# Optimization experiments

Hardware: AMD Instinct MI355X
Metric: run time of the kernel (lower is better)

The kernel has to match this reference:

```python
import jax, jax.numpy as jnp
import numpy as np

B, S, H, NH, L, INTER, WIN = 2, 2048, 512, 8, 4, 2048, 64
HD = H // NH
W1 = WIN // 2          # one-sided window
WB = 2 * W1 + 1        # band width per query
EPS = 1e-12


def layer_norm(x, g, b):
    m = jnp.mean(x, axis=-1, keepdims=True)
    v = jnp.var(x, axis=-1, keepdims=True)
    return (x - m) / jnp.sqrt(v + EPS) * g + b


def setup_inputs() -> dict:
    key = jax.random.key(0)
    ks = jax.random.split(key, 12)
    std = 0.02
    n = lambda k, sh: jax.random.normal(k, sh, jnp.float32) * std
    return {
        "input_embs": jax.random.normal(ks[0], (B, S, H), jnp.float32),
        "attention_mask": jnp.ones((B, S), jnp.float32),
        "pos_emb": n(ks[1], (S, H)),
        "ln_emb_g": jnp.ones((H,), jnp.float32),
        "ln_emb_b": jnp.zeros((H,), jnp.float32),
        "Wq": n(ks[2], (L, H, H)), "bq": jnp.zeros((L, H), jnp.float32),
        "Wk": n(ks[3], (L, H, H)), "bk": jnp.zeros((L, H), jnp.float32),
        "Wv": n(ks[4], (L, H, H)), "bv": jnp.zeros((L, H), jnp.float32),
        "Wo": n(ks[5], (L, H, H)), "bo": jnp.zeros((L, H), jnp.float32),
        "ln1_g": jnp.ones((L, H), jnp.float32), "ln1_b": jnp.zeros((L, H), jnp.float32),
        "Wi": n(ks[6], (L, H, INTER)), "bi": jnp.zeros((L, INTER), jnp.float32),
        "Wo2": n(ks[7], (L, INTER, H)), "bo2": jnp.zeros((L, H), jnp.float32),
        "ln2_g": jnp.ones((L, H), jnp.float32), "ln2_b": jnp.zeros((L, H), jnp.float32),
        "pool_W1": n(ks[8], (H, H)), "pool_b1": jnp.zeros((H,), jnp.float32),
        "pool_W2": n(ks[9], (H, 1)), "pool_b2": jnp.zeros((1,), jnp.float32),
    }


def reference(input_embs, attention_mask, pos_emb, ln_emb_g, ln_emb_b,
              Wq, bq, Wk, bk, Wv, bv, Wo, bo, ln1_g, ln1_b,
              Wi, bi, Wo2, bo2, ln2_g, ln2_b,
              pool_W1, pool_b1, pool_W2, pool_b2):
    # extended additive mask: 0 for attend, -10000 for pad (no global tokens)
    ext = (1.0 - attention_mask) * -10000.0          # [B,S]
    is_masked = ext < 0                              # masked query positions

    # embeddings: input + position, LayerNorm (dropout is identity in eval)
    x = layer_norm(input_embs + pos_emb[None], ln_emb_g, ln_emb_b)

    # sliding-window band indices
    offs = jnp.arange(-W1, W1 + 1)
    idx = jnp.arange(S)[:, None] + offs[None, :]     # [S,WB]
    valid = (idx >= 0) & (idx < S)
    idxc = jnp.clip(idx, 0, S - 1)
    key_bias = ext[:, idxc]                          # [B,S,WB] additive key mask
    scale = 1.0 / jnp.sqrt(jnp.float32(HD))

    def layer(h, p):
        (wq, bq_, wk, bk_, wv, bv_, wo, bo_, g1, b1,
         wi, bi_, wo2, bo2_, g2, b2) = p
        q = (h @ wq + bq_).reshape(B, S, NH, HD) * scale
        k = (h @ wk + bk_).reshape(B, S, NH, HD)
        v = (h @ wv + bv_).reshape(B, S, NH, HD)
        kb = k[:, idxc]                              # [B,S,WB,NH,HD]
        vb = v[:, idxc]
        sc = jnp.einsum('bshd,bswhd->bhsw', q, kb) + key_bias[:, None]
        sc = jnp.where(valid[None, None], sc, -jnp.inf)
        pr = jax.nn.softmax(sc, axis=-1)
        pr = jnp.where(is_masked[:, None, :, None], 0.0, pr)
        ctx = jnp.einsum('bhsw,bswhd->bshd', pr, vb).reshape(B, S, H)
        attn = layer_norm(ctx @ wo + bo_ + h, g1, b1)          # BertSelfOutput
        inter = jax.nn.gelu(attn @ wi + bi_, approximate=False)  # BertIntermediate
        out = layer_norm(inter @ wo2 + bo2_ + attn, g2, b2)      # BertOutput
        return out, None

    params = (Wq, bq, Wk, bk, Wv, bv, Wo, bo, ln1_g, ln1_b,
              Wi, bi, Wo2, bo2, ln2_g, ln2_b)
    x, _ = jax.lax.scan(jax.checkpoint(layer), x, params)

    # AttentionPooling
    e = jnp.tanh(x @ pool_W1 + pool_b1)
    alpha = jnp.exp(e @ pool_W2 + pool_b2) * attention_mask[..., None]  # [B,S,1]
    alpha = alpha / (jnp.sum(alpha, axis=1, keepdims=True) + 1e-8)
    return jnp.einsum('bsh,bs->bh', x, alpha[..., 0])  # [B,H]
```

## Files before the change

### kernel.cpp

```cpp
#include <hip/hip_runtime.h>
#include <hip/hip_bf16.h>
#include <math.h>

#define B_ 2
#define S_ 2048
#define H_ 512
#define NH_ 8
#define HD_ 64
#define L_ 4
#define INTER_ 2048
#define W1_ 32
#define WB_ 65
#define M_ (B_*S_)

typedef __attribute__((ext_vector_type(8))) short short8v;
typedef __attribute__((ext_vector_type(4))) float f32x4;

__device__ __forceinline__ float b2f(ushort u){ return __uint_as_float(((unsigned)u)<<16); }
__device__ __forceinline__ ushort f2b(float f){
  unsigned u = __float_as_uint(f);
  unsigned r = (u + 0x7fffu + ((u>>16)&1u)) >> 16;
  return (ushort)r;
}

__device__ __forceinline__ void async16(const ushort* g, ushort* l){
  __builtin_amdgcn_global_load_lds(
      (const __attribute__((address_space(1))) unsigned int*)g,
      (__attribute__((address_space(3))) unsigned int*)l, 16, 0, 0);
}

__global__ __launch_bounds__(256) void transpose_k(const float* __restrict__ src,
    ushort* __restrict__ dst, int R, int C, size_t sBatch, size_t dBatch)
{
  __shared__ ushort tile[32][33];
  src += (size_t)blockIdx.z * sBatch;
  dst += (size_t)blockIdx.z * dBatch;
  int tx = threadIdx.x & 31, ty = threadIdx.x >> 5;
  int r0 = blockIdx.y * 32, c0 = blockIdx.x * 32;
  #pragma unroll
  for (int i = 0; i < 4; ++i){
    int r = r0 + ty + i*8;
    tile[ty + i*8][tx] = f2b(src[(size_t)r * C + c0 + tx]);
  }
  __syncthreads();
  #pragma unroll
  for (int i = 0; i < 4; ++i){
    int c = c0 + ty + i*8;
    dst[(size_t)c * R + r0 + tx] = tile[tx][ty + i*8];
  }
}

__global__ __launch_bounds__(256) void pack_bqkv(const float* __restrict__ bq,
    const float* __restrict__ bk, const float* __restrict__ bv, float* __restrict__ dst)
{
  int i = blockIdx.x * 256 + threadIdx.x;
  int l = i / 1536, n = i % 1536;
  float v = (n < 512) ? bq[l*512 + n] : (n < 1024 ? bk[l*512 + n - 512] : bv[l*512 + n - 1024]);
  dst[i] = v;
}

template<int EPI>
__global__ __launch_bounds__(256, 4) void gemm_bt(
    const ushort* __restrict__ A, const ushort* __restrict__ Bt,
    const float* __restrict__ bias, ushort* __restrict__ o16,
    float* __restrict__ o32, int M, int N, int K)
{
  __shared__ ushort lds_a[64][32];
  __shared__ ushort lds_b[128][32];
  const int tid = threadIdx.x;
  const int bm = blockIdx.y * 64, bn = blockIdx.x * 128;
  const int wave = tid >> 6, lane = tid & 63;
  const int wr = (wave >> 1) * 32, wc = (wave & 1) * 64;
  const int lr = lane & 15, lg = lane >> 4, lk = lg * 8;
  f32x4 acc[2][4] = {};

  const int srow = tid >> 2, schk = (tid & 3) * 8;
  const ushort* Ag  = A  + (size_t)(bm + srow) * K + schk;
  const ushort* Bg0 = Bt + (size_t)(bn + srow) * K + schk;
  const ushort* Bg1 = Bt + (size_t)(bn + 64 + srow) * K + schk;
  ushort* la  = &lds_a[0][0] + tid * 8;
  ushort* lb0 = &lds_b[0][0] + tid * 8;
  ushort* lb1 = &lds_b[64][0] + tid * 8;

  for (int k0 = 0; k0 < K; k0 += 32){
    __syncthreads();
    async16(Ag  + k0, la);
    async16(Bg0 + k0, lb0);
    async16(Bg1 + k0, lb1);
    __syncthreads();
    short8v af[2], bfr[4];
    #pragma unroll
    for (int mi = 0; mi < 2; ++mi)
      af[mi] = *(const short8v*)(&lds_a[wr + mi*16 + lr][lk]);
    #pragma unroll
    for (int nj = 0; nj < 4; ++nj)
      bfr[nj] = *(const short8v*)(&lds_b[wc + nj*16 + lr][lk]);
    #pragma unroll
    for (int mi = 0; mi < 2; ++mi)
      #pragma unroll
      for (int nj = 0; nj < 4; ++nj)
        acc[mi][nj] = __builtin_amdgcn_mfma_f32_16x16x32_bf16(af[mi], bfr[nj], acc[mi][nj], 0, 0, 0);
  }

  #pragma unroll
  for (int mi = 0; mi < 2; ++mi){
    #pragma unroll
    for (int nj = 0; nj < 4; ++nj){
      int col = bn + wc + nj*16 + lr;
      float bv = bias[col];
      #pragma unroll
      for (int j = 0; j < 4; ++j){
        int row = bm + wr + mi*16 + lg*4 + j;
        float v = acc[mi][nj][j] + bv;
        if (EPI == 1) v = 0.5f * v * (1.0f + erff(v * 0.70710678118654752f));
        if (EPI == 2) v = tanhf(v);
        if (EPI == 3) o32[(size_t)row * N + col] = v;
        else          o16[(size_t)row * N + col] = f2b(v);
      }
    }
  }
}

__device__ __forceinline__ void block_ln_stats(float v0, float v1, float* red,
                                               float& mean, float& rstd)
{
  int tid = threadIdx.x, wave = tid >> 6, lane = tid & 63;
  float sm = v0 + v1;
  float sq = v0*v0 + v1*v1;
  #pragma unroll
  for (int o = 32; o > 0; o >>= 1){ sm += __shfl_xor(sm, o); sq += __shfl_xor(sq, o); }
  if (lane == 0){ red[wave] = sm; red[4 + wave] = sq; }
  __syncthreads();
  float S = red[0] + red[1] + red[2] + red[3];
  float Q = red[4] + red[5] + red[6] + red[7];
  mean = S * (1.0f / 512.0f);
  float var = Q * (1.0f / 512.0f) - mean*mean;
  if (var < 0.f) var = 0.f;
  rstd = rsqrtf(var + 1e-12f);
}

__global__ __launch_bounds__(256) void embed_ln(const float* __restrict__ x,
    const float* __restrict__ pos, const float* __restrict__ g,
    const float* __restrict__ bb, ushort* __restrict__ out16, float* __restrict__ out32)
{
  __shared__ float red[8];
  int row = blockIdx.x, tid = threadIdx.x;
  int s = row & (S_ - 1);
  float v0 = x[(size_t)row*H_ + tid]       + pos[(size_t)s*H_ + tid];
  float v1 = x[(size_t)row*H_ + tid + 256] + pos[(size_t)s*H_ + tid + 256];
  float mean, rstd;
  block_ln_stats(v0, v1, red, mean, rstd);
  float r0 = (v0 - mean)*rstd*g[tid]       + bb[tid];
  float r1 = (v1 - mean)*rstd*g[tid + 256] + bb[tid + 256];
  out16[(size_t)row*H_ + tid]       = f2b(r0);
  out16[(size_t)row*H_ + tid + 256] = f2b(r1);
  out32[(size_t)row*H_ + tid]       = r0;
  out32[(size_t)row*H_ + tid + 256] = r1;
}

__global__ __launch_bounds__(256) void ln_res(const float* __restrict__ t,
    const float* __restrict__ res, const float* __restrict__ g,
    const float* __restrict__ bb, ushort* __restrict__ out16, float* __restrict__ out32)
{
  __shared__ float red[8];
  int row = blockIdx.x, tid = threadIdx.x;
  float v0 = t[(size_t)row*H_ + tid]       + res[(size_t)row*H_ + tid];
  float v1 = t[(size_t)row*H_ + tid + 256] + res[(size_t)row*H_ + tid + 256];
  float mean, rstd;
  block_ln_stats(v0, v1, red, mean, rstd);
  float r0 = (v0 - mean)*rstd*g[tid]       + bb[tid];
  float r1 = (v1 - mean)*rstd*g[tid + 256] + bb[tid + 256];
  out16[(size_t)row*H_ + tid]       = f2b(r0);
  out16[(size_t)row*H_ + tid + 256] = f2b(r1);
  out32[(size_t)row*H_ + tid]       = r0;
  out32[(size_t)row*H_ + tid + 256] = r1;
}

__global__ __launch_bounds__(256) void attn_mfma(const ushort* __restrict__ qkv,
    const float* __restrict__ mask, ushort* __restrict__ ctx)
{
  __shared__ ushort K_lds[128][72];
  __shared__ ushort Vt[64][136];
  __shared__ ushort P_lds[64][136];
  __shared__ float  kb[128];

  const int tid = threadIdx.x, wave = tid >> 6, lane = tid & 63;
  const int hh = blockIdx.y & (NH_ - 1), b = blockIdx.y >> 3;
  const int s0 = blockIdx.x * 64;
  const size_t rb = (size_t)b * S_;

  const int ch = tid & 7;
  const int rr = tid >> 3;
  #pragma unroll
  for (int it = 0; it < 4; ++it){
    int c = rr + it*32;
    int j = s0 - 32 + c;
    int jc = min(max(j, 0), S_ - 1);
    const size_t rowb = (rb + jc) * 1536 + hh*64 + ch*8;
    *(short8v*)(&K_lds[c][ch*8]) = *(const short8v*)(qkv + rowb + 512);
    short8v vv = *(const short8v*)(qkv + rowb + 1024);
    #pragma unroll
    for (int t = 0; t < 8; ++t){
      int tt = (t + ch) & 7;
      Vt[ch*8 + tt][c] = (ushort)vv[tt];
    }
  }
  if (tid < 128){
    int j = s0 - 32 + tid;
    kb[tid] = (j >= 0 && j < S_) ? (1.0f - mask[rb + j]) * (-10000.0f) : -1e30f;
  }
  __syncthreads();

  const int wq0 = wave * 16;
  const int lr = lane & 15, lg = lane >> 4, lk = lg * 8;

  const ushort* qbase = qkv + (rb + s0 + wq0 + lr) * 1536 + hh*64;
  short8v aq0 = *(const short8v*)(qbase + lk);
  short8v aq1 = *(const short8v*)(qbase + 32 + lk);

  f32x4 sacc[8];
  #pragma unroll
  for (int cn = 0; cn < 8; ++cn){
    short8v bk0 = *(const short8v*)(&K_lds[cn*16 + lr][lk]);
    short8v bk1 = *(const short8v*)(&K_lds[cn*16 + lr][32 + lk]);
    f32x4 z = {0.f, 0.f, 0.f, 0.f};
    z = __builtin_amdgcn_mfma_f32_16x16x32_bf16(aq0, bk0, z, 0, 0, 0);
    z = __builtin_amdgcn_mfma_f32_16x16x32_bf16(aq1, bk1, z, 0, 0, 0);
    sacc[cn] = z;
  }

  #pragma unroll
  for (int jr = 0; jr < 4; ++jr){
    const int R = wq0 + lg*4 + jr;
    float v[8], mx = -1e30f;
    #pragma unroll
    for (int cn = 0; cn < 8; ++cn){
      int c = cn*16 + lr;
      float sc = sacc[cn][jr] * 0.125f + kb[c];
      if (c < R || c > R + 64) sc = -1e30f;
      v[cn] = sc;
      mx = fmaxf(mx, sc);
    }
    #pragma unroll
    for (int o = 1; o < 16; o <<= 1) mx = fmaxf(mx, __shfl_xor(mx, o));
    float sum = 0.f;
    #pragma unroll
    for (int cn = 0; cn < 8; ++cn){ v[cn] = __expf(v[cn] - mx); sum += v[cn]; }
    #pragma unroll
    for (int o = 1; o < 16; o <<= 1) sum += __shfl_xor(sum, o);
    float qm = mask[rb + s0 + R];
    float inv = ((qm < 0.999f) ? 0.0f : 1.0f) / sum;
    #pragma unroll
    for (int cn = 0; cn < 8; ++cn)
      P_lds[R][cn*16 + lr] = f2b(v[cn] * inv);
  }

  short8v ap[4];
  #pragma unroll
  for (int ks = 0; ks < 4; ++ks)
    ap[ks] = *(const short8v*)(&P_lds[wq0 + lr][ks*32 + lk]);
  #pragma unroll
  for (int dn = 0; dn < 4; ++dn){
    f32x4 z = {0.f, 0.f, 0.f, 0.f};
    #pragma unroll
    for (int ks = 0; ks < 4; ++ks){
      short8v bv = *(const short8v*)(&Vt[dn*16 + lr][ks*32 + lk]);
      z = __builtin_amdgcn_mfma_f32_16x16x32_bf16(ap[ks], bv, z, 0, 0, 0);
    }
    #pragma unroll
    for (int jr = 0; jr < 4; ++jr){
      int R = wq0 + lg*4 + jr;
      ctx[(rb + s0 + R)*H_ + hh*64 + dn*16 + lr] = f2b(z[jr]);
    }
  }
}

__global__ __launch_bounds__(256) void pool_logit(const ushort* __restrict__ e,
    const float* __restrict__ w2, const float* __restrict__ b2p,
    const float* __restrict__ mask, float* __restrict__ alpha)
{
  int tid = threadIdx.x, wave = tid >> 6, lane = tid & 63;
  int r = blockIdx.x * 4 + wave;
  short8v ev = *(const short8v*)(e + (size_t)r*H_ + lane*8);
  float sacc = 0.f;
  #pragma unroll
  for (int j = 0; j < 8; ++j) sacc += b2f((ushort)ev[j]) * w2[lane*8 + j];
  #pragma unroll
  for (int o = 32; o > 0; o >>= 1) sacc += __shfl_xor(sacc, o);
  if (lane == 0){
    float logit = sacc + b2p[0];
    alpha[r] = __expf(logit) * mask[r];
  }
}

__global__ __launch_bounds__(256) void pool_sum(const float* __restrict__ alpha,
                                                float* __restrict__ invsum)
{
  __shared__ float red[4];
  int b = blockIdx.x, tid = threadIdx.x, wave = tid >> 6, lane = tid & 63;
  float s = 0.f;
  for (int k = tid; k < S_; k += 256) s += alpha[b*S_ + k];
  #pragma unroll
  for (int o = 32; o > 0; o >>= 1) s += __shfl_xor(s, o);
  if (lane == 0) red[wave] = s;
  __syncthreads();
  if (tid == 0) invsum[b] = 1.0f / (red[0] + red[1] + red[2] + red[3] + 1e-8f);
}

__global__ __launch_bounds__(256) void pool_wsum(const float* __restrict__ x,
    const float* __restrict__ alpha, float* __restrict__ out_acc)
{
  int chunk = blockIdx.x, b = blockIdx.y, tid = threadIdx.x;
  int s0 = chunk * 128;
  float a0 = 0.f, a1 = 0.f;
  for (int i = 0; i < 128; ++i){
    int srow = s0 + i;
    float al = alpha[b*S_ + srow];
    a0 += x[(size_t)(b*S_ + srow)*H_ + tid]       * al;
    a1 += x[(size_t)(b*S_ + srow)*H_ + tid + 256] * al;
  }
  out_acc[(size_t)chunk*B_*H_ + b*H_ + tid]       = a0;
  out_acc[(size_t)chunk*B_*H_ + b*H_ + tid + 256] = a1;
}

__global__ __launch_bounds__(256) void pool_final(const float* __restrict__ out_acc,
    const float* __restrict__ invsum, float* __restrict__ out)
{
  int i = blockIdx.x * 256 + threadIdx.x;
  if (i < B_*H_){
    int b = i >> 9;
    float s = 0.f;
    #pragma unroll
    for (int c = 0; c < 16; ++c) s += out_acc[(size_t)c*B_*H_ + i];
    out[i] = s * invsum[b];
  }
}

extern "C" void kernel_launch(void* const* d_in, const int* in_sizes, int n_in,
                              void* d_out, int out_size, void* d_ws, size_t ws_size,
                              hipStream_t stream)
{
  const float* input_embs = (const float*)d_in[0];
  const float* mask       = (const float*)d_in[1];
  const float* pos        = (const float*)d_in[2];
  const float* ln_emb_g   = (const float*)d_in[3];
  const float* ln_emb_b   = (const float*)d_in[4];
  const float* Wq  = (const float*)d_in[5];
  const float* bq  = (const float*)d_in[6];
  const float* Wk  = (const float*)d_in[7];
  const float* bk  = (const float*)d_in[8];
  const float* Wv  = (const float*)d_in[9];
  const float* bv  = (const float*)d_in[10];
  const float* Wo  = (const float*)d_in[11];
  const float* bo  = (const float*)d_in[12];
  const float* ln1_g = (const float*)d_in[13];
  const float* ln1_b = (const float*)d_in[14];
  const float* Wi  = (const float*)d_in[15];
  const float* bi  = (const float*)d_in[16];
  const float* Wo2 = (const float*)d_in[17];
  const float* bo2 = (const float*)d_in[18];
  const float* ln2_g = (const float*)d_in[19];
  const float* ln2_b = (const float*)d_in[20];
  const float* pW1 = (const float*)d_in[21];
  const float* pb1 = (const float*)d_in[22];
  const float* pW2 = (const float*)d_in[23];
  const float* pb2 = (const float*)d_in[24];

  char* ws = (char*)d_ws;
  size_t off = 0;
  auto alloc = [&](size_t bytes)->char*{
    char* p = ws + off; off += (bytes + 255) & ~(size_t)255; return p;
  };
  ushort* WqkvT  = (ushort*)alloc((size_t)L_*1536*512*2);
  ushort* WoT    = (ushort*)alloc((size_t)L_*512*512*2);
  ushort* WiT    = (ushort*)alloc((size_t)L_*2048*512*2);
  ushort* Wo2T   = (ushort*)alloc((size_t)L_*512*2048*2);
  ushort* pW1T   = (ushort*)alloc((size_t)512*512*2);
  float*  bqkv   = (float*)alloc((size_t)L_*1536*4);
  ushort* h16    = (ushort*)alloc((size_t)M_*H_*2);
  float*  h32    = (float*)alloc((size_t)M_*H_*4);
  ushort* qkv    = (ushort*)alloc((size_t)M_*1536*2);
  ushort* ctx    = (ushort*)alloc((size_t)M_*H_*2);
  ushort* attn16 = (ushort*)alloc((size_t)M_*H_*2);
  float*  attn32 = (float*)alloc((size_t)M_*H_*4);
  ushort* inter  = (ushort*)alloc((size_t)M_*INTER_*2);
  float*  t1     = (float*)alloc((size_t)M_*H_*4);
  float*  alpha  = (float*)alloc((size_t)M_*4);
  float*  invsum = (float*)alloc(256);
  float*  outacc = (float*)alloc((size_t)16*B_*H_*4);

  dim3 tb(256);
  transpose_k<<<dim3(16,16,L_), tb, 0, stream>>>(Wq, WqkvT,            512,  512, (size_t)512*512,  (size_t)1536*512);
  transpose_k<<<dim3(16,16,L_), tb, 0, stream>>>(Wk, WqkvT + 512*512,  512,  512, (size_t)512*512,  (size_t)1536*512);
  transpose_k<<<dim3(16,16,L_), tb, 0, stream>>>(Wv, WqkvT + 1024*512, 512,  512, (size_t)512*512,  (size_t)1536*512);
  transpose_k<<<dim3(16,16,L_), tb, 0, stream>>>(Wo, WoT,              512,  512, (size_t)512*512,  (size_t)512*512);
  transpose_k<<<dim3(64,16,L_), tb, 0, stream>>>(Wi, WiT,              512, 2048, (size_t)512*2048, (size_t)2048*512);
  transpose_k<<<dim3(16,64,L_), tb, 0, stream>>>(Wo2, Wo2T,           2048,  512, (size_t)2048*512, (size_t)512*2048);
  transpose_k<<<dim3(16,16,1),  tb, 0, stream>>>(pW1, pW1T,            512,  512, 0, 0);
  pack_bqkv<<<dim3(L_*1536/256), tb, 0, stream>>>(bq, bk, bv, bqkv);

  embed_ln<<<dim3(M_), tb, 0, stream>>>(input_embs, pos, ln_emb_g, ln_emb_b, h16, h32);

  for (int l = 0; l < L_; ++l){
    gemm_bt<0><<<dim3(12,64), tb, 0, stream>>>(h16, WqkvT + (size_t)l*1536*512, bqkv + l*1536,
                                               qkv, nullptr, M_, 1536, 512);
    attn_mfma<<<dim3(S_/64, B_*NH_), tb, 0, stream>>>(qkv, mask, ctx);
    gemm_bt<3><<<dim3(4,64), tb, 0, stream>>>(ctx, WoT + (size_t)l*512*512, bo + l*512,
                                              nullptr, t1, M_, 512, 512);
    ln_res<<<dim3(M_), tb, 0, stream>>>(t1, h32, ln1_g + l*512, ln1_b + l*512, attn16, attn32);
    gemm_bt<1><<<dim3(16,64), tb, 0, stream>>>(attn16, WiT + (size_t)l*2048*512, bi + l*2048,
                                               inter, nullptr, M_, 2048, 512);
    gemm_bt<3><<<dim3(4,64), tb, 0, stream>>>(inter, Wo2T + (size_t)l*512*2048, bo2 + l*512,
                                              nullptr, t1, M_, 512, 2048);
    ln_res<<<dim3(M_), tb, 0, stream>>>(t1, attn32, ln2_g + l*512, ln2_b + l*512, h16, h32);
  }

  gemm_bt<2><<<dim3(4,64), tb, 0, stream>>>(h16, pW1T, pb1, ctx, nullptr, M_, 512, 512);
  pool_logit<<<dim3(M_/4), tb, 0, stream>>>(ctx, pW2, pb2, mask, alpha);
  pool_sum<<<dim3(B_), tb, 0, stream>>>(alpha, invsum);
  pool_wsum<<<dim3(16, B_), tb, 0, stream>>>(h32, alpha, outacc);
  pool_final<<<dim3((B_*H_ + 255)/256), tb, 0, stream>>>(outacc, invsum, (float*)d_out);
}
```

Baseline: 475.6 us.

## Double-buffer GEMM LDS tiles and split-K the N=512 projections

The GEMM now keeps two LDS buffers, so the next K-tile's async loads are issued while MFMAs run on the current tile, and each iteration needs one barrier instead of two. The N=512 output projections (Wo and Wo2) are split along K into two z-slices that write separate fp32 partials; only the first slice adds the bias, and ln_res sums both partials before the residual add. This is meant to hide global load latency and to double the block count of the under-filled 256-block GEMMs. In exchange it doubles LDS use, adds an extra fp32 partial buffer with more write and read traffic, and ln_res now always reads two partials.

After: 440.8 us. -7.3%, faster.

```diff
diff --git a/kernel.cpp b/kernel.cpp
--- a/kernel.cpp
+++ b/kernel.cpp
@@ -63,58 +63,70 @@
 __global__ __launch_bounds__(256, 4) void gemm_bt(
     const ushort* __restrict__ A, const ushort* __restrict__ Bt,
     const float* __restrict__ bias, ushort* __restrict__ o16,
-    float* __restrict__ o32, int M, int N, int K)
-{
-  __shared__ ushort lds_a[64][32];
-  __shared__ ushort lds_b[128][32];
+    float* __restrict__ o32, int M, int N, int K, int Klen)
+{
+  __shared__ ushort lds_a[2][64][32];
+  __shared__ ushort lds_b[2][128][32];
   const int tid = threadIdx.x;
   const int bm = blockIdx.y * 64, bn = blockIdx.x * 128;
+  const int kbeg = blockIdx.z * Klen;
   const int wave = tid >> 6, lane = tid & 63;
   const int wr = (wave >> 1) * 32, wc = (wave & 1) * 64;
   const int lr = lane & 15, lg = lane >> 4, lk = lg * 8;
   f32x4 acc[2][4] = {};
 
   const int srow = tid >> 2, schk = (tid & 3) * 8;
-  const ushort* Ag  = A  + (size_t)(bm + srow) * K + schk;
-  const ushort* Bg0 = Bt + (size_t)(bn + srow) * K + schk;
-  const ushort* Bg1 = Bt + (size_t)(bn + 64 + srow) * K + schk;
-  ushort* la  = &lds_a[0][0] + tid * 8;
-  ushort* lb0 = &lds_b[0][0] + tid * 8;
-  ushort* lb1 = &lds_b[64][0] + tid * 8;
-
-  for (int k0 = 0; k0 < K; k0 += 32){
-    __syncthreads();
-    async16(Ag  + k0, la);
-    async16(Bg0 + k0, lb0);
-    async16(Bg1 + k0, lb1);
-    __syncthreads();
+  const ushort* Ag  = A  + (size_t)(bm + srow) * K + kbeg + schk;
+  const ushort* Bg0 = Bt + (size_t)(bn + srow) * K + kbeg + schk;
+  const ushort* Bg1 = Bt + (size_t)(bn + 64 + srow) * K + kbeg + schk;
+  ushort* la = &lds_a[0][0][0] + tid * 8;
+  ushort* lb = &lds_b[0][0][0] + tid * 8;
+
+  const int nIter = Klen >> 5;
+  async16(Ag, la);
+  async16(Bg0, lb);
+  async16(Bg1, lb + 2048);
+  __syncthreads();
+
+  int cur = 0;
+  for (int t = 0; t < nIter; ++t){
+    if (t + 1 < nIter){
+      int k0 = (t + 1) << 5;
+      int nb = cur ^ 1;
+      async16(Ag  + k0, la + nb*2048);
+      async16(Bg0 + k0, lb + nb*4096);
+      async16(Bg1 + k0, lb + nb*4096 + 2048);
+    }
     short8v af[2], bfr[4];
     #pragma unroll
     for (int mi = 0; mi < 2; ++mi)
-      af[mi] = *(const short8v*)(&lds_a[wr + mi*16 + lr][lk]);
+      af[mi] = *(const short8v*)(&lds_a[cur][wr + mi*16 + lr][lk]);
     #pragma unroll
     for (int nj = 0; nj < 4; ++nj)
-      bfr[nj] = *(const short8v*)(&lds_b[wc + nj*16 + lr][lk]);
+      bfr[nj] = *(const short8v*)(&lds_b[cur][wc + nj*16 + lr][lk]);
     #pragma unroll
     for (int mi = 0; mi < 2; ++mi)
       #pragma unroll
       for (int nj = 0; nj < 4; ++nj)
         acc[mi][nj] = __builtin_amdgcn_mfma_f32_16x16x32_bf16(af[mi], bfr[nj], acc[mi][nj], 0, 0, 0);
-  }
-
+    __syncthreads();
+    cur ^= 1;
+  }
+
+  const float bscale = (blockIdx.z == 0) ? 1.0f : 0.0f;
   #pragma unroll
   for (int mi = 0; mi < 2; ++mi){
     #pragma unroll
     for (int nj = 0; nj < 4; ++nj){
       int col = bn + wc + nj*16 + lr;
-      float bv = bias[col];
+      float bv = bias[col] * bscale;
       #pragma unroll
       for (int j = 0; j < 4; ++j){
         int row = bm + wr + mi*16 + lg*4 + j;
         float v = acc[mi][nj][j] + bv;
         if (EPI == 1) v = 0.5f * v * (1.0f + erff(v * 0.70710678118654752f));
         if (EPI == 2) v = tanhf(v);
-        if (EPI == 3) o32[(size_t)row * N + col] = v;
+        if (EPI == 3) o32[(size_t)blockIdx.z*M*N + (size_t)row * N + col] = v;
         else          o16[(size_t)row * N + col] = f2b(v);
       }
     }
@@ -164,8 +176,11 @@
 {
   __shared__ float red[8];
   int row = blockIdx.x, tid = threadIdx.x;
-  float v0 = t[(size_t)row*H_ + tid]       + res[(size_t)row*H_ + tid];
-  float v1 = t[(size_t)row*H_ + tid + 256] + res[(size_t)row*H_ + tid + 256];
+  const size_t MN = (size_t)M_*H_;
+  float v0 = t[(size_t)row*H_ + tid]       + t[MN + (size_t)row*H_ + tid]
+           + res[(size_t)row*H_ + tid];
+  float v1 = t[(size_t)row*H_ + tid + 256] + t[MN + (size_t)row*H_ + tid + 256]
+           + res[(size_t)row*H_ + tid + 256];
   float mean, rstd;
   block_ln_stats(v0, v1, red, mean, rstd);
   float r0 = (v0 - mean)*rstd*g[tid]       + bb[tid];
@@ -384,7 +399,7 @@
   ushort* attn16 = (ushort*)alloc((size_t)M_*H_*2);
   float*  attn32 = (float*)alloc((size_t)M_*H_*4);
   ushort* inter  = (ushort*)alloc((size_t)M_*INTER_*2);
-  float*  t1     = (float*)alloc((size_t)M_*H_*4);
+  float*  t1     = (float*)alloc((size_t)2*M_*H_*4);
   float*  alpha  = (float*)alloc((size_t)M_*4);
   float*  invsum = (float*)alloc(256);
   float*  outacc = (float*)alloc((size_t)16*B_*H_*4);
@@ -402,20 +417,20 @@
   embed_ln<<<dim3(M_), tb, 0, stream>>>(input_embs, pos, ln_emb_g, ln_emb_b, h16, h32);
 
   for (int l = 0; l < L_; ++l){
-    gemm_bt<0><<<dim3(12,64), tb, 0, stream>>>(h16, WqkvT + (size_t)l*1536*512, bqkv + l*1536,
-                                               qkv, nullptr, M_, 1536, 512);
+    gemm_bt<0><<<dim3(12,64,1), tb, 0, stream>>>(h16, WqkvT + (size_t)l*1536*512, bqkv + l*1536,
+                                                 qkv, nullptr, M_, 1536, 512, 512);
     attn_mfma<<<dim3(S_/64, B_*NH_), tb, 0, stream>>>(qkv, mask, ctx);
-    gemm_bt<3><<<dim3(4,64), tb, 0, stream>>>(ctx, WoT + (size_t)l*512*512, bo + l*512,
-                                              nullptr, t1, M_, 512, 512);
+    gemm_bt<3><<<dim3(4,64,2), tb, 0, stream>>>(ctx, WoT + (size_t)l*512*512, bo + l*512,
+                                                nullptr, t1, M_, 512, 512, 256);
     ln_res<<<dim3(M_), tb, 0, stream>>>(t1, h32, ln1_g + l*512, ln1_b + l*512, attn16, attn32);
-    gemm_bt<1><<<dim3(16,64), tb, 0, stream>>>(attn16, WiT + (size_t)l*2048*512, bi + l*2048,
-                                               inter, nullptr, M_, 2048, 512);
-    gemm_bt<3><<<dim3(4,64), tb, 0, stream>>>(inter, Wo2T + (size_t)l*512*2048, bo2 + l*512,
-                                              nullptr, t1, M_, 512, 2048);
+    gemm_bt<1><<<dim3(16,64,1), tb, 0, stream>>>(attn16, WiT + (size_t)l*2048*512, bi + l*2048,
+                                                 inter, nullptr, M_, 2048, 512, 512);
+    gemm_bt<3><<<dim3(4,64,2), tb, 0, stream>>>(inter, Wo2T + (size_t)l*512*2048, bo2 + l*512,
+                                                nullptr, t1, M_, 512, 2048, 1024);
     ln_res<<<dim3(M_), tb, 0, stream>>>(t1, attn32, ln2_g + l*512, ln2_b + l*512, h16, h32);
   }
 
-  gemm_bt<2><<<dim3(4,64), tb, 0, stream>>>(h16, pW1T, pb1, ctx, nullptr, M_, 512, 512);
+  gemm_bt<2><<<dim3(4,64,1), tb, 0, stream>>>(h16, pW1T, pb1, ctx, nullptr, M_, 512, 512, 512);
   pool_logit<<<dim3(M_/4), tb, 0, stream>>>(ctx, pW2, pb2, mask, alpha);
   pool_sum<<<dim3(B_), tb, 0, stream>>>(alpha, invsum);
   pool_wsum<<<dim3(16, B_), tb, 0, stream>>>(h32, alpha, outacc);
```
